# Optimization experiments

Hardware: AMD Instinct MI355X
Metric: run time of the kernel (lower is better)

## Reference

```python
import jax, jax.numpy as jnp
import numpy as np

B, T, D, U = 32, 1024, 512, 512

def hard_sigmoid(x):
    # Keras hard_sigmoid: clip(0.2*x + 0.5, 0, 1)
    return jnp.clip(x * 0.2 + 0.5, 0.0, 1.0)

def setup_inputs() -> dict:
    key = jax.random.key(0)
    k1, k2, k3 = jax.random.split(key, 3)
    x = jax.random.normal(k1, (B, T, D), dtype=jnp.float32)
    kernel = jax.random.normal(k2, (D, 4 * U), dtype=jnp.float32) * 0.02
    recurrent_kernel = jax.random.normal(k3, (U, 4 * U), dtype=jnp.float32) * 0.02
    # unit_forget_bias: forget-gate slice initialized to 1
    bias = jnp.zeros((4 * U,), dtype=jnp.float32).at[U:2 * U].set(1.0)
    return {"x": x, "kernel": kernel, "recurrent_kernel": recurrent_kernel, "bias": bias}

def reference(x, kernel, recurrent_kernel, bias):
    units = recurrent_kernel.shape[0]
    batch = x.shape[0]
    # Precompute input projections for all timesteps in one big GEMM
    # (implementation=2 style): [B, T, 4U]
    xz = jnp.einsum('btd,dg->btg', x, kernel) + bias
    xz_t = jnp.transpose(xz, (1, 0, 2))  # [T, B, 4U]

    h0 = jnp.zeros((batch, units), dtype=x.dtype)
    c0 = jnp.zeros((batch, units), dtype=x.dtype)

    def step(carry, z_x):
        h, c = carry
        z = z_x + h @ recurrent_kernel  # [B, 4U]
        zi, zf, zc, zo = jnp.split(z, 4, axis=-1)
        i = hard_sigmoid(zi)
        f = hard_sigmoid(zf)
        c_new = f * c + i * jnp.tanh(zc)
        o = hard_sigmoid(zo)
        h_new = o * jnp.tanh(c_new)
        return (h_new, c_new), h_new

    (_, _), hs = jax.lax.scan(step, (h0, c0), xz_t)  # hs: [T, B, U]
    return jnp.transpose(hs, (1, 0, 2))  # [B, T, U] (return_sequences=True)
```

## Files before the change

### kernel.cpp

```cpp
#include <hip/hip_runtime.h>


#define TT 1024
#define DD 512
#define UU 512
#define NCOL 2048
#define SENT 0xFFFFFFFFu
#define RDEPTH 4

typedef float f32x2 __attribute__((ext_vector_type(2)));
typedef float f32x4 __attribute__((ext_vector_type(4)));

__device__ __forceinline__ float hsig(float v) {
  return fminf(fmaxf(0.2f * v + 0.5f, 0.0f), 1.0f);
}
__device__ __forceinline__ float tanh_fast(float x) {
  float e = __expf(2.0f * x);
  return 1.0f - 2.0f / (e + 1.0f);
}

template <bool SLEEP>
__device__ __forceinline__ void wavebar(int* ctr, int& ep) {
  asm volatile("s_waitcnt lgkmcnt(0)" ::: "memory");
  if ((threadIdx.x & 63) == 0)
    __hip_atomic_fetch_add(ctr, 1, __ATOMIC_RELAXED, __HIP_MEMORY_SCOPE_WORKGROUP);
  ep += 4;
  while (__hip_atomic_load(ctr, __ATOMIC_RELAXED, __HIP_MEMORY_SCOPE_WORKGROUP) < ep) {
    if (SLEEP) __builtin_amdgcn_s_sleep(1);
  }
  asm volatile("" ::: "memory");
}

__global__ __launch_bounds__(512, 2) void lstm_persistent(
    const float* __restrict__ x,
    const float* __restrict__ Wk,
    const float* __restrict__ Wr,
    const float* __restrict__ bias,
    float* __restrict__ out) {
  const int tid = (int)threadIdx.x;
  const int g   = (int)blockIdx.x & 7;
  const int w   = (int)blockIdx.x >> 3;
  const bool crit = (tid < 256);
  const int l   = tid & 63;

  __shared__ float LX[8][4][65];
  __shared__ float LR[2][8][4][66];
  __shared__ float RING[RDEPTH][4][66];
  __shared__ float LH[4][8][68];
  __shared__ float LB[64];
  __shared__ int cXZdone, cCRITdone, cXZbar, cCRITbar;

  if (tid == 0) { cXZdone = 0; cCRITdone = 0; cXZbar = 0; cCRITbar = 0; }
  if (tid < 64) LB[tid] = bias[(tid >> 4) * UU + w * 16 + (tid & 15)];

  f32x2 W2[64];
  {
    const int wv  = tid >> 6;
    const int idx = tid & 255;
    const int cp  = crit ? (l & 31) : (idx & 31);
    const int ko  = crit ? (2 * (wv & 3) + (l >> 5)) : (idx >> 5);
    const int gcb = (cp >> 3) * UU + w * 16 + ((2 * cp) & 15);
    const float* M = crit ? Wr : Wk;
#pragma unroll
    for (int j = 0; j < 64; ++j)
      W2[j] = *(const f32x2*)(M + (size_t)(64 * ko + j) * NCOL + gcb);
  }
  __syncthreads();

  if (crit) {
    const int wv  = tid >> 6;
    const int kq0 = 2 * wv;
    const int kql = kq0 + (l >> 5);
    const int cp  = l & 31;
    const unsigned* ou0 = (const unsigned*)out + (size_t)(g * 4 + 0) * TT * UU;
    const unsigned* ou1 = (const unsigned*)out + (size_t)(g * 4 + 1) * TT * UU;
    const unsigned* ou2 = (const unsigned*)out + (size_t)(g * 4 + 2) * TT * UU;
    const unsigned* ou3 = (const unsigned*)out + (size_t)(g * 4 + 3) * TT * UU;
    float c_state = 0.0f;
    int epC = 0;

    for (int t = 0; t < TT; ++t) {
      if (t > 0) {
        const size_t roff = (size_t)(t - 1) * UU + 128 * wv + l;
        unsigned v0, v1, v2, v3, v4, v5, v6, v7;
        for (;;) {
          v0 = __hip_atomic_load(ou0 + roff,      __ATOMIC_RELAXED, __HIP_MEMORY_SCOPE_AGENT);
          v1 = __hip_atomic_load(ou0 + roff + 64, __ATOMIC_RELAXED, __HIP_MEMORY_SCOPE_AGENT);
          v2 = __hip_atomic_load(ou1 + roff,      __ATOMIC_RELAXED, __HIP_MEMORY_SCOPE_AGENT);
          v3 = __hip_atomic_load(ou1 + roff + 64, __ATOMIC_RELAXED, __HIP_MEMORY_SCOPE_AGENT);
          v4 = __hip_atomic_load(ou2 + roff,      __ATOMIC_RELAXED, __HIP_MEMORY_SCOPE_AGENT);
          v5 = __hip_atomic_load(ou2 + roff + 64, __ATOMIC_RELAXED, __HIP_MEMORY_SCOPE_AGENT);
          v6 = __hip_atomic_load(ou3 + roff,      __ATOMIC_RELAXED, __HIP_MEMORY_SCOPE_AGENT);
          v7 = __hip_atomic_load(ou3 + roff + 64, __ATOMIC_RELAXED, __HIP_MEMORY_SCOPE_AGENT);
          int ok = (v0 != SENT) & (v1 != SENT) & (v2 != SENT) & (v3 != SENT) &
                   (v4 != SENT) & (v5 != SENT) & (v6 != SENT) & (v7 != SENT);
          if (__all(ok)) break;
          __builtin_amdgcn_s_sleep(1);
        }
        LH[0][kq0    ][l] = __uint_as_float(v0);
        LH[0][kq0 + 1][l] = __uint_as_float(v1);
        LH[1][kq0    ][l] = __uint_as_float(v2);
        LH[1][kq0 + 1][l] = __uint_as_float(v3);
        LH[2][kq0    ][l] = __uint_as_float(v4);
        LH[2][kq0 + 1][l] = __uint_as_float(v5);
        LH[3][kq0    ][l] = __uint_as_float(v6);
        LH[3][kq0 + 1][l] = __uint_as_float(v7);
        asm volatile("s_waitcnt lgkmcnt(0)" ::: "memory");
        __builtin_amdgcn_sched_barrier(0);
        __builtin_amdgcn_s_setprio(1);
        f32x2 a0 = {0.f, 0.f}, a1 = {0.f, 0.f}, a2 = {0.f, 0.f}, a3 = {0.f, 0.f};
#pragma unroll
        for (int j4 = 0; j4 < 16; ++j4) {
          f32x4 h0 = *(const f32x4*)&LH[0][kql][4 * j4];
          f32x4 h1 = *(const f32x4*)&LH[1][kql][4 * j4];
          f32x4 h2 = *(const f32x4*)&LH[2][kql][4 * j4];
          f32x4 h3 = *(const f32x4*)&LH[3][kql][4 * j4];
#pragma unroll
          for (int jj = 0; jj < 4; ++jj) {
            f32x2 wj = W2[4 * j4 + jj];
            a0 += (f32x2){h0[jj], h0[jj]} * wj;
            a1 += (f32x2){h1[jj], h1[jj]} * wj;
            a2 += (f32x2){h2[jj], h2[jj]} * wj;
            a3 += (f32x2){h3[jj], h3[jj]} * wj;
          }
        }
        __builtin_amdgcn_s_setprio(0);
        const int p = t & 1;
        *(f32x2*)&LR[p][kql][0][2 * cp] = a0;
        *(f32x2*)&LR[p][kql][1][2 * cp] = a1;
        *(f32x2*)&LR[p][kql][2][2 * cp] = a2;
        *(f32x2*)&LR[p][kql][3][2 * cp] = a3;
      }
      float s0 = 0.f, s1 = 0.f, s2 = 0.f, s3 = 0.f;
      if (l < 16) {
        while (__hip_atomic_load(&cXZdone, __ATOMIC_RELAXED,
                                 __HIP_MEMORY_SCOPE_WORKGROUP) < t + 1) {
        }
        asm volatile("" ::: "memory");
        const int ss = t & (RDEPTH - 1);
        s0 = RING[ss][wv][l +  0] + LB[l +  0];
        s1 = RING[ss][wv][l + 16] + LB[l + 16];
        s2 = RING[ss][wv][l + 32] + LB[l + 32];
        s3 = RING[ss][wv][l + 48] + LB[l + 48];
      }
      wavebar<false>(&cCRITbar, epC);
      if (l == 0)
        __hip_atomic_fetch_add(&cCRITdone, 1, __ATOMIC_RELAXED,
                               __HIP_MEMORY_SCOPE_WORKGROUP);
      if (l < 16) {
        if (t > 0) {
          const int p = t & 1;
#pragma unroll
          for (int kq = 0; kq < 8; ++kq) {
            s0 += LR[p][kq][wv][l +  0];
            s1 += LR[p][kq][wv][l + 16];
            s2 += LR[p][kq][wv][l + 32];
            s3 += LR[p][kq][wv][l + 48];
          }
        }
        float gi = hsig(s0);
        float gf = hsig(s1);
        float gc = tanh_fast(s2);
        float go = hsig(s3);
        c_state = gf * c_state + gi * gc;
        float h = go * tanh_fast(c_state);
        __hip_atomic_store(
            out + ((size_t)(g * 4 + wv) * TT + t) * UU + w * 16 + l, h,
            __ATOMIC_RELAXED, __HIP_MEMORY_SCOPE_AGENT);
      }
    }
  } else {
    const int idx = tid & 255;
    const int o   = idx >> 5;
    const int cp  = idx & 31;
    const float* xb0 = x + (size_t)(g * 4 + 0) * TT * DD + o * 64;
    const float* xb1 = x + (size_t)(g * 4 + 1) * TT * DD + o * 64;
    const float* xb2 = x + (size_t)(g * 4 + 2) * TT * DD + o * 64;
    const float* xb3 = x + (size_t)(g * 4 + 3) * TT * DD + o * 64;
    int epX = 0;

    for (int t = 0; t < TT; ++t) {
      const size_t off = (size_t)t * DD;
      f32x2 a0 = {0.f, 0.f}, a1 = {0.f, 0.f}, a2 = {0.f, 0.f}, a3 = {0.f, 0.f};
#pragma unroll
      for (int j4 = 0; j4 < 16; ++j4) {
        f32x4 v0 = *(const f32x4*)(xb0 + off + 4 * j4);
        f32x4 v1 = *(const f32x4*)(xb1 + off + 4 * j4);
        f32x4 v2 = *(const f32x4*)(xb2 + off + 4 * j4);
        f32x4 v3 = *(const f32x4*)(xb3 + off + 4 * j4);
#pragma unroll
        for (int jj = 0; jj < 4; ++jj) {
          f32x2 wj = W2[4 * j4 + jj];
          a0 += (f32x2){v0[jj], v0[jj]} * wj;
          a1 += (f32x2){v1[jj], v1[jj]} * wj;
          a2 += (f32x2){v2[jj], v2[jj]} * wj;
          a3 += (f32x2){v3[jj], v3[jj]} * wj;
        }
      }
      *(f32x2*)&LX[o][0][2 * cp] = a0;
      *(f32x2*)&LX[o][1][2 * cp] = a1;
      *(f32x2*)&LX[o][2][2 * cp] = a2;
      *(f32x2*)&LX[o][3][2 * cp] = a3;
      wavebar<true>(&cXZbar, epX);
      if (t >= RDEPTH) {
        while (__hip_atomic_load(&cCRITdone, __ATOMIC_RELAXED,
                                 __HIP_MEMORY_SCOPE_WORKGROUP) <
               4 * (t - RDEPTH + 1)) {
          __builtin_amdgcn_s_sleep(1);
        }
        asm volatile("" ::: "memory");
      }
      {
        const int b2 = idx >> 6, c3 = idx & 63;
        float ssum = 0.f;
#pragma unroll
        for (int oo = 0; oo < 8; ++oo) ssum += LX[oo][b2][c3];
        RING[t & (RDEPTH - 1)][b2][c3] = ssum;
      }
      wavebar<true>(&cXZbar, epX);
      if (idx == 0) {
        asm volatile("s_waitcnt lgkmcnt(0)" ::: "memory");
        __hip_atomic_fetch_add(&cXZdone, 1, __ATOMIC_RELAXED,
                               __HIP_MEMORY_SCOPE_WORKGROUP);
      }
    }
  }
}

extern "C" void kernel_launch(void* const* d_in, const int* in_sizes, int n_in,
                              void* d_out, int out_size, void* d_ws, size_t ws_size,
                              hipStream_t stream) {
  const float* x    = (const float*)d_in[0];
  const float* Wk   = (const float*)d_in[1];
  const float* Wr   = (const float*)d_in[2];
  const float* bias = (const float*)d_in[3];
  float* out = (float*)d_out;

  hipMemsetAsync(out, 0xFF, (size_t)out_size * sizeof(float), stream);
  lstm_persistent<<<256, 512, 0, stream>>>(x, Wk, Wr, bias, out);
}
```

Before: 4.274 ms.

## Interleave two batch groups per block to hide recurrent step latency

Each block now alternates between two batch groups (q and q^1) inside each timestep. It keeps separate cell state, ring buffers and progress counters per group, and halves the input-projection ring depth. The intent is to overlap the global-memory wait on one group's hidden state with compute for the other group. The grid is unchanged, so partner blocks compute and write identical results for the same group pair. Per-block work and barriers roughly double, and the two groups' step chains are serialised within the block.

```diff
diff --git a/kernel.cpp b/kernel.cpp
--- a/kernel.cpp
+++ b/kernel.cpp
@@ -6,7 +6,7 @@
 #define UU 512
 #define NCOL 2048
 #define SENT 0xFFFFFFFFu
-#define RDEPTH 4
+#define RDEPTH 2
 
 typedef float f32x2 __attribute__((ext_vector_type(2)));
 typedef float f32x4 __attribute__((ext_vector_type(4)));
@@ -38,20 +38,23 @@
     const float* __restrict__ bias,
     float* __restrict__ out) {
   const int tid = (int)threadIdx.x;
-  const int g   = (int)blockIdx.x & 7;
-  const int w   = (int)blockIdx.x >> 3;
+  const int i   = (int)blockIdx.x;
+  const int u   = i >> 3;
+  const int q   = i & 7;
+  const int grp[2] = {q, q ^ 1};
   const bool crit = (tid < 256);
   const int l   = tid & 63;
 
   __shared__ float LX[8][4][65];
   __shared__ float LR[2][8][4][66];
-  __shared__ float RING[RDEPTH][4][66];
+  __shared__ float RING[2][RDEPTH][4][66];
   __shared__ float LH[4][8][68];
   __shared__ float LB[64];
-  __shared__ int cXZdone, cCRITdone, cXZbar, cCRITbar;
-
-  if (tid == 0) { cXZdone = 0; cCRITdone = 0; cXZbar = 0; cCRITbar = 0; }
-  if (tid < 64) LB[tid] = bias[(tid >> 4) * UU + w * 16 + (tid & 15)];
+  __shared__ int cXZdone[2], cCRITdone[2], cXZbar, cCRITbar;
+
+  if (tid < 2) { cXZdone[tid] = 0; cCRITdone[tid] = 0; }
+  if (tid == 0) { cXZbar = 0; cCRITbar = 0; }
+  if (tid < 64) LB[tid] = bias[(tid >> 4) * UU + u * 16 + (tid & 15)];
 
   f32x2 W2[64];
   {
@@ -59,7 +62,7 @@
     const int idx = tid & 255;
     const int cp  = crit ? (l & 31) : (idx & 31);
     const int ko  = crit ? (2 * (wv & 3) + (l >> 5)) : (idx >> 5);
-    const int gcb = (cp >> 3) * UU + w * 16 + ((2 * cp) & 15);
+    const int gcb = (cp >> 3) * UU + u * 16 + ((2 * cp) & 15);
     const float* M = crit ? Wr : Wk;
 #pragma unroll
     for (int j = 0; j < 64; ++j)
@@ -72,156 +75,164 @@
     const int kq0 = 2 * wv;
     const int kql = kq0 + (l >> 5);
     const int cp  = l & 31;
-    const unsigned* ou0 = (const unsigned*)out + (size_t)(g * 4 + 0) * TT * UU;
-    const unsigned* ou1 = (const unsigned*)out + (size_t)(g * 4 + 1) * TT * UU;
-    const unsigned* ou2 = (const unsigned*)out + (size_t)(g * 4 + 2) * TT * UU;
-    const unsigned* ou3 = (const unsigned*)out + (size_t)(g * 4 + 3) * TT * UU;
-    float c_state = 0.0f;
+    float c_state[2] = {0.0f, 0.0f};
     int epC = 0;
+    const unsigned* oub[2][4];
+#pragma unroll
+    for (int ph = 0; ph < 2; ++ph)
+#pragma unroll
+      for (int k = 0; k < 4; ++k)
+        oub[ph][k] = (const unsigned*)out + (size_t)(grp[ph] * 4 + k) * TT * UU;
 
     for (int t = 0; t < TT; ++t) {
-      if (t > 0) {
-        const size_t roff = (size_t)(t - 1) * UU + 128 * wv + l;
-        unsigned v0, v1, v2, v3, v4, v5, v6, v7;
-        for (;;) {
-          v0 = __hip_atomic_load(ou0 + roff,      __ATOMIC_RELAXED, __HIP_MEMORY_SCOPE_AGENT);
-          v1 = __hip_atomic_load(ou0 + roff + 64, __ATOMIC_RELAXED, __HIP_MEMORY_SCOPE_AGENT);
-          v2 = __hip_atomic_load(ou1 + roff,      __ATOMIC_RELAXED, __HIP_MEMORY_SCOPE_AGENT);
-          v3 = __hip_atomic_load(ou1 + roff + 64, __ATOMIC_RELAXED, __HIP_MEMORY_SCOPE_AGENT);
-          v4 = __hip_atomic_load(ou2 + roff,      __ATOMIC_RELAXED, __HIP_MEMORY_SCOPE_AGENT);
-          v5 = __hip_atomic_load(ou2 + roff + 64, __ATOMIC_RELAXED, __HIP_MEMORY_SCOPE_AGENT);
-          v6 = __hip_atomic_load(ou3 + roff,      __ATOMIC_RELAXED, __HIP_MEMORY_SCOPE_AGENT);
-          v7 = __hip_atomic_load(ou3 + roff + 64, __ATOMIC_RELAXED, __HIP_MEMORY_SCOPE_AGENT);
-          int ok = (v0 != SENT) & (v1 != SENT) & (v2 != SENT) & (v3 != SENT) &
-                   (v4 != SENT) & (v5 != SENT) & (v6 != SENT) & (v7 != SENT);
-          if (__all(ok)) break;
-          __builtin_amdgcn_s_sleep(1);
-        }
-        LH[0][kq0    ][l] = __uint_as_float(v0);
-        LH[0][kq0 + 1][l] = __uint_as_float(v1);
-        LH[1][kq0    ][l] = __uint_as_float(v2);
-        LH[1][kq0 + 1][l] = __uint_as_float(v3);
-        LH[2][kq0    ][l] = __uint_as_float(v4);
-        LH[2][kq0 + 1][l] = __uint_as_float(v5);
-        LH[3][kq0    ][l] = __uint_as_float(v6);
-        LH[3][kq0 + 1][l] = __uint_as_float(v7);
-        asm volatile("s_waitcnt lgkmcnt(0)" ::: "memory");
-        __builtin_amdgcn_sched_barrier(0);
-        __builtin_amdgcn_s_setprio(1);
-        f32x2 a0 = {0.f, 0.f}, a1 = {0.f, 0.f}, a2 = {0.f, 0.f}, a3 = {0.f, 0.f};
-#pragma unroll
-        for (int j4 = 0; j4 < 16; ++j4) {
-          f32x4 h0 = *(const f32x4*)&LH[0][kql][4 * j4];
-          f32x4 h1 = *(const f32x4*)&LH[1][kql][4 * j4];
-          f32x4 h2 = *(const f32x4*)&LH[2][kql][4 * j4];
-          f32x4 h3 = *(const f32x4*)&LH[3][kql][4 * j4];
-#pragma unroll
-          for (int jj = 0; jj < 4; ++jj) {
-            f32x2 wj = W2[4 * j4 + jj];
-            a0 += (f32x2){h0[jj], h0[jj]} * wj;
-            a1 += (f32x2){h1[jj], h1[jj]} * wj;
-            a2 += (f32x2){h2[jj], h2[jj]} * wj;
-            a3 += (f32x2){h3[jj], h3[jj]} * wj;
-          }
-        }
-        __builtin_amdgcn_s_setprio(0);
-        const int p = t & 1;
-        *(f32x2*)&LR[p][kql][0][2 * cp] = a0;
-        *(f32x2*)&LR[p][kql][1][2 * cp] = a1;
-        *(f32x2*)&LR[p][kql][2][2 * cp] = a2;
-        *(f32x2*)&LR[p][kql][3][2 * cp] = a3;
-      }
-      float s0 = 0.f, s1 = 0.f, s2 = 0.f, s3 = 0.f;
-      if (l < 16) {
-        while (__hip_atomic_load(&cXZdone, __ATOMIC_RELAXED,
-                                 __HIP_MEMORY_SCOPE_WORKGROUP) < t + 1) {
-        }
-        asm volatile("" ::: "memory");
-        const int ss = t & (RDEPTH - 1);
-        s0 = RING[ss][wv][l +  0] + LB[l +  0];
-        s1 = RING[ss][wv][l + 16] + LB[l + 16];
-        s2 = RING[ss][wv][l + 32] + LB[l + 32];
-        s3 = RING[ss][wv][l + 48] + LB[l + 48];
-      }
-      wavebar<false>(&cCRITbar, epC);
-      if (l == 0)
-        __hip_atomic_fetch_add(&cCRITdone, 1, __ATOMIC_RELAXED,
-                               __HIP_MEMORY_SCOPE_WORKGROUP);
-      if (l < 16) {
+#pragma unroll
+      for (int ph = 0; ph < 2; ++ph) {
         if (t > 0) {
-          const int p = t & 1;
-#pragma unroll
-          for (int kq = 0; kq < 8; ++kq) {
-            s0 += LR[p][kq][wv][l +  0];
-            s1 += LR[p][kq][wv][l + 16];
-            s2 += LR[p][kq][wv][l + 32];
-            s3 += LR[p][kq][wv][l + 48];
-          }
-        }
-        float gi = hsig(s0);
-        float gf = hsig(s1);
-        float gc = tanh_fast(s2);
-        float go = hsig(s3);
-        c_state = gf * c_state + gi * gc;
-        float h = go * tanh_fast(c_state);
-        __hip_atomic_store(
-            out + ((size_t)(g * 4 + wv) * TT + t) * UU + w * 16 + l, h,
-            __ATOMIC_RELAXED, __HIP_MEMORY_SCOPE_AGENT);
+          const size_t roff = (size_t)(t - 1) * UU + 128 * wv + l;
+          unsigned v0, v1, v2, v3, v4, v5, v6, v7;
+          for (;;) {
+            v0 = __hip_atomic_load(oub[ph][0] + roff,      __ATOMIC_RELAXED, __HIP_MEMORY_SCOPE_AGENT);
+            v1 = __hip_atomic_load(oub[ph][0] + roff + 64, __ATOMIC_RELAXED, __HIP_MEMORY_SCOPE_AGENT);
+            v2 = __hip_atomic_load(oub[ph][1] + roff,      __ATOMIC_RELAXED, __HIP_MEMORY_SCOPE_AGENT);
+            v3 = __hip_atomic_load(oub[ph][1] + roff + 64, __ATOMIC_RELAXED, __HIP_MEMORY_SCOPE_AGENT);
+            v4 = __hip_atomic_load(oub[ph][2] + roff,      __ATOMIC_RELAXED, __HIP_MEMORY_SCOPE_AGENT);
+            v5 = __hip_atomic_load(oub[ph][2] + roff + 64, __ATOMIC_RELAXED, __HIP_MEMORY_SCOPE_AGENT);
+            v6 = __hip_atomic_load(oub[ph][3] + roff,      __ATOMIC_RELAXED, __HIP_MEMORY_SCOPE_AGENT);
+            v7 = __hip_atomic_load(oub[ph][3] + roff + 64, __ATOMIC_RELAXED, __HIP_MEMORY_SCOPE_AGENT);
+            int ok = (v0 != SENT) & (v1 != SENT) & (v2 != SENT) & (v3 != SENT) &
+                     (v4 != SENT) & (v5 != SENT) & (v6 != SENT) & (v7 != SENT);
+            if (__all(ok)) break;
+            __builtin_amdgcn_s_sleep(1);
+          }
+          LH[0][kq0    ][l] = __uint_as_float(v0);
+          LH[0][kq0 + 1][l] = __uint_as_float(v1);
+          LH[1][kq0    ][l] = __uint_as_float(v2);
+          LH[1][kq0 + 1][l] = __uint_as_float(v3);
+          LH[2][kq0    ][l] = __uint_as_float(v4);
+          LH[2][kq0 + 1][l] = __uint_as_float(v5);
+          LH[3][kq0    ][l] = __uint_as_float(v6);
+          LH[3][kq0 + 1][l] = __uint_as_float(v7);
+          asm volatile("s_waitcnt lgkmcnt(0)" ::: "memory");
+          __builtin_amdgcn_sched_barrier(0);
+          __builtin_amdgcn_s_setprio(1);
+          f32x2 a0 = {0.f, 0.f}, a1 = {0.f, 0.f}, a2 = {0.f, 0.f}, a3 = {0.f, 0.f};
+#pragma unroll
+          for (int j4 = 0; j4 < 16; ++j4) {
+            f32x4 h0 = *(const f32x4*)&LH[0][kql][4 * j4];
+            f32x4 h1 = *(const f32x4*)&LH[1][kql][4 * j4];
+            f32x4 h2 = *(const f32x4*)&LH[2][kql][4 * j4];
+            f32x4 h3 = *(const f32x4*)&LH[3][kql][4 * j4];
+#pragma unroll
+            for (int jj = 0; jj < 4; ++jj) {
+              f32x2 wj = W2[4 * j4 + jj];
+              a0 += (f32x2){h0[jj], h0[jj]} * wj;
+              a1 += (f32x2){h1[jj], h1[jj]} * wj;
+              a2 += (f32x2){h2[jj], h2[jj]} * wj;
+              a3 += (f32x2){h3[jj], h3[jj]} * wj;
+            }
+          }
+          __builtin_amdgcn_s_setprio(0);
+          *(f32x2*)&LR[ph][kql][0][2 * cp] = a0;
+          *(f32x2*)&LR[ph][kql][1][2 * cp] = a1;
+          *(f32x2*)&LR[ph][kql][2][2 * cp] = a2;
+          *(f32x2*)&LR[ph][kql][3][2 * cp] = a3;
+        }
+        float s0 = 0.f, s1 = 0.f, s2 = 0.f, s3 = 0.f;
+        if (l < 16) {
+          while (__hip_atomic_load(&cXZdone[ph], __ATOMIC_RELAXED,
+                                   __HIP_MEMORY_SCOPE_WORKGROUP) < t + 1) {
+          }
+          asm volatile("" ::: "memory");
+          const int ss = t & (RDEPTH - 1);
+          s0 = RING[ph][ss][wv][l +  0] + LB[l +  0];
+          s1 = RING[ph][ss][wv][l + 16] + LB[l + 16];
+          s2 = RING[ph][ss][wv][l + 32] + LB[l + 32];
+          s3 = RING[ph][ss][wv][l + 48] + LB[l + 48];
+        }
+        wavebar<false>(&cCRITbar, epC);
+        if (l == 0)
+          __hip_atomic_fetch_add(&cCRITdone[ph], 1, __ATOMIC_RELAXED,
+                                 __HIP_MEMORY_SCOPE_WORKGROUP);
+        if (l < 16) {
+          if (t > 0) {
+#pragma unroll
+            for (int kq = 0; kq < 8; ++kq) {
+              s0 += LR[ph][kq][wv][l +  0];
+              s1 += LR[ph][kq][wv][l + 16];
+              s2 += LR[ph][kq][wv][l + 32];
+              s3 += LR[ph][kq][wv][l + 48];
+            }
+          }
+          float gi = hsig(s0);
+          float gf = hsig(s1);
+          float gc = tanh_fast(s2);
+          float go = hsig(s3);
+          c_state[ph] = gf * c_state[ph] + gi * gc;
+          float h = go * tanh_fast(c_state[ph]);
+          __hip_atomic_store(
+              out + ((size_t)(grp[ph] * 4 + wv) * TT + t) * UU + u * 16 + l, h,
+              __ATOMIC_RELAXED, __HIP_MEMORY_SCOPE_AGENT);
+        }
       }
     }
   } else {
     const int idx = tid & 255;
     const int o   = idx >> 5;
     const int cp  = idx & 31;
-    const float* xb0 = x + (size_t)(g * 4 + 0) * TT * DD + o * 64;
-    const float* xb1 = x + (size_t)(g * 4 + 1) * TT * DD + o * 64;
-    const float* xb2 = x + (size_t)(g * 4 + 2) * TT * DD + o * 64;
-    const float* xb3 = x + (size_t)(g * 4 + 3) * TT * DD + o * 64;
     int epX = 0;
+    const float* xb[2][4];
+#pragma unroll
+    for (int ph = 0; ph < 2; ++ph)
+#pragma unroll
+      for (int k = 0; k < 4; ++k)
+        xb[ph][k] = x + (size_t)(grp[ph] * 4 + k) * TT * DD + o * 64;
 
     for (int t = 0; t < TT; ++t) {
-      const size_t off = (size_t)t * DD;
-      f32x2 a0 = {0.f, 0.f}, a1 = {0.f, 0.f}, a2 = {0.f, 0.f}, a3 = {0.f, 0.f};
-#pragma unroll
-      for (int j4 = 0; j4 < 16; ++j4) {
-        f32x4 v0 = *(const f32x4*)(xb0 + off + 4 * j4);
-        f32x4 v1 = *(const f32x4*)(xb1 + off + 4 * j4);
-        f32x4 v2 = *(const f32x4*)(xb2 + off + 4 * j4);
-        f32x4 v3 = *(const f32x4*)(xb3 + off + 4 * j4);
-#pragma unroll
-        for (int jj = 0; jj < 4; ++jj) {
-          f32x2 wj = W2[4 * j4 + jj];
-          a0 += (f32x2){v0[jj], v0[jj]} * wj;
-          a1 += (f32x2){v1[jj], v1[jj]} * wj;
-          a2 += (f32x2){v2[jj], v2[jj]} * wj;
-          a3 += (f32x2){v3[jj], v3[jj]} * wj;
-        }
-      }
-      *(f32x2*)&LX[o][0][2 * cp] = a0;
-      *(f32x2*)&LX[o][1][2 * cp] = a1;
-      *(f32x2*)&LX[o][2][2 * cp] = a2;
-      *(f32x2*)&LX[o][3][2 * cp] = a3;
-      wavebar<true>(&cXZbar, epX);
-      if (t >= RDEPTH) {
-        while (__hip_atomic_load(&cCRITdone, __ATOMIC_RELAXED,
-                                 __HIP_MEMORY_SCOPE_WORKGROUP) <
-               4 * (t - RDEPTH + 1)) {
-          __builtin_amdgcn_s_sleep(1);
-        }
-        asm volatile("" ::: "memory");
-      }
-      {
-        const int b2 = idx >> 6, c3 = idx & 63;
-        float ssum = 0.f;
-#pragma unroll
-        for (int oo = 0; oo < 8; ++oo) ssum += LX[oo][b2][c3];
-        RING[t & (RDEPTH - 1)][b2][c3] = ssum;
-      }
-      wavebar<true>(&cXZbar, epX);
-      if (idx == 0) {
-        asm volatile("s_waitcnt lgkmcnt(0)" ::: "memory");
-        __hip_atomic_fetch_add(&cXZdone, 1, __ATOMIC_RELAXED,
-                               __HIP_MEMORY_SCOPE_WORKGROUP);
+#pragma unroll
+      for (int ph = 0; ph < 2; ++ph) {
+        const size_t off = (size_t)t * DD;
+        f32x2 a0 = {0.f, 0.f}, a1 = {0.f, 0.f}, a2 = {0.f, 0.f}, a3 = {0.f, 0.f};
+#pragma unroll
+        for (int j4 = 0; j4 < 16; ++j4) {
+          f32x4 v0 = *(const f32x4*)(xb[ph][0] + off + 4 * j4);
+          f32x4 v1 = *(const f32x4*)(xb[ph][1] + off + 4 * j4);
+          f32x4 v2 = *(const f32x4*)(xb[ph][2] + off + 4 * j4);
+          f32x4 v3 = *(const f32x4*)(xb[ph][3] + off + 4 * j4);
+#pragma unroll
+          for (int jj = 0; jj < 4; ++jj) {
+            f32x2 wj = W2[4 * j4 + jj];
+            a0 += (f32x2){v0[jj], v0[jj]} * wj;
+            a1 += (f32x2){v1[jj], v1[jj]} * wj;
+            a2 += (f32x2){v2[jj], v2[jj]} * wj;
+            a3 += (f32x2){v3[jj], v3[jj]} * wj;
+          }
+        }
+        *(f32x2*)&LX[o][0][2 * cp] = a0;
+        *(f32x2*)&LX[o][1][2 * cp] = a1;
+        *(f32x2*)&LX[o][2][2 * cp] = a2;
+        *(f32x2*)&LX[o][3][2 * cp] = a3;
+        wavebar<true>(&cXZbar, epX);
+        if (t >= RDEPTH) {
+          while (__hip_atomic_load(&cCRITdone[ph], __ATOMIC_RELAXED,
+                                   __HIP_MEMORY_SCOPE_WORKGROUP) <
+                 4 * (t - RDEPTH + 1)) {
+            __builtin_amdgcn_s_sleep(1);
+          }
+          asm volatile("" ::: "memory");
+        }
+        {
+          const int b2 = idx >> 6, c3 = idx & 63;
+          float ssum = 0.f;
+#pragma unroll
+          for (int oo = 0; oo < 8; ++oo) ssum += LX[oo][b2][c3];
+          RING[ph][t & (RDEPTH - 1)][b2][c3] = ssum;
+        }
+        wavebar<true>(&cXZbar, epX);
+        if (idx == 0) {
+          asm volatile("s_waitcnt lgkmcnt(0)" ::: "memory");
+          __hip_atomic_fetch_add(&cXZdone[ph], 1, __ATOMIC_RELAXED,
+                                 __HIP_MEMORY_SCOPE_WORKGROUP);
+        }
       }
     }
   }
```

Result: slower. 6.108 ms (+42.9%).
